# Kernel optimization log

Measured on AMD Instinct MI355X. Metric: run time of the kernel, lower is better.

Reference implementation:

```python
import jax, jax.numpy as jnp
import numpy as np
from jax import lax

T, H, K, V, O = 8192, 2048, 512, 512, 2048


def setup_inputs() -> dict:
    key = jax.random.key(0)
    ks = jax.random.split(key, 11)
    s_h = 1.0 / np.sqrt(H)
    s_v = 1.0 / np.sqrt(V)
    return {
        "hidden_state": jax.random.normal(ks[0], (T, H), jnp.float32),
        "Wq": jax.random.normal(ks[1], (H, K), jnp.float32) * s_h,
        "bq": jax.random.normal(ks[2], (K,), jnp.float32) * 0.02,
        "Wk": jax.random.normal(ks[3], (H, K), jnp.float32) * s_h,
        "bk": jax.random.normal(ks[4], (K,), jnp.float32) * 0.02,
        "Wv": jax.random.normal(ks[5], (H, V), jnp.float32) * s_h,
        "bv": jax.random.normal(ks[6], (V,), jnp.float32) * 0.02,
        "Wg": jax.random.normal(ks[7], (H, K), jnp.float32) * s_h,
        "bg": jax.random.normal(ks[8], (K,), jnp.float32) * 0.02,
        "Wo": jax.random.normal(ks[9], (V, O), jnp.float32) * s_v,
        "bo": jax.random.normal(ks[10], (O,), jnp.float32) * 0.02,
    }


def reference(hidden_state, Wq, bq, Wk, bk, Wv, bv, Wg, bg, Wo, bo):
    # Batched projections (torch Linear: x @ W^T + b; here W stored as [in,out])
    q = hidden_state @ Wq + bq                    # [T, K]
    k = jax.nn.sigmoid(hidden_state @ Wk + bk)    # [T, K]
    g = jax.nn.sigmoid(hidden_state @ Wg + bg)    # [T, K]
    v = hidden_state @ Wv + bv                    # [T, V]

    def step(state, qkvg):
        qi, ki, vi, gi = qkvg
        # state: [K, V]; gated decay per key-dim row, then outer-product write
        state = state * gi[:, None] + ki[:, None] * vi[None, :]
        out_i = qi @ state  # == state.T @ qi -> [V]
        return state, out_i

    init = jnp.zeros((K, V), hidden_state.dtype)
    final_state, outs = lax.scan(step, init, (q, k, v, g))  # outs: [T, V]
    output = outs @ Wo + bo                                  # [T, O]
    return output, final_state
```

## Files before the change

### kernel.cpp

```cpp
#include <hip/hip_runtime.h>

#define T_LEN 8192
#define H_DIM 2048
#define K_DIM 512
#define V_DIM 512
#define O_DIM 2048
#define CHUNK 64
#define NCHUNK 128

typedef short bf16x8 __attribute__((ext_vector_type(8)));
typedef float f32x4 __attribute__((ext_vector_type(4)));

typedef const __attribute__((address_space(1))) void* gptr1_t;
typedef __attribute__((address_space(3))) void* lptr3_t;

__device__ __forceinline__ float b2f(unsigned short u) {
    unsigned int i = ((unsigned int)u) << 16;
    float f;
    __builtin_memcpy(&f, &i, 4);
    return f;
}
__device__ __forceinline__ unsigned short f2b(float f) {
    unsigned int i;
    __builtin_memcpy(&i, &f, 4);
    unsigned int r = (i + 0x7FFFu + ((i >> 16) & 1u)) >> 16;
    return (unsigned short)r;
}
__device__ __forceinline__ float fw(float v) {
    return fminf(fmaxf(v, -1e30f), 1e30f);
}

#define BARX() asm volatile("s_barrier" ::: "memory")

__global__ __launch_bounds__(64) void probe_k(int* __restrict__ flag) {
    __shared__ unsigned short As[16 * 32];
    __shared__ unsigned short Bs[16 * 32];
    int tid = threadIdx.x;
    for (int idx = tid; idx < 512; idx += 64) {
        int r = idx >> 5, c = idx & 31;
        float av = (c == 0) ? (float)(r + 1) : (c == 1 ? 1.0f : 0.0f);
        float bv = (c == 0) ? 1.0f : (c == 1 ? (float)(1024 * (r + 1)) : 0.0f);
        As[r * 32 + c] = f2b(av);
        Bs[r * 32 + c] = f2b(bv);
    }
    __syncthreads();
    int ln15 = tid & 15, q4 = (tid & 63) >> 4;
    bf16x8 a = *(const bf16x8*)(As + ln15 * 32 + q4 * 8);
    bf16x8 b = *(const bf16x8*)(Bs + ln15 * 32 + q4 * 8);
    f32x4 acc = {0.f, 0.f, 0.f, 0.f};
    acc = __builtin_amdgcn_mfma_f32_16x16x32_bf16(a, b, acc, 0, 0, 0);
    bool h0 = true, h1 = true;
#pragma unroll
    for (int i = 0; i < 4; i++) {
        float e0 = (float)((q4 * 4 + i + 1) + 1024 * (ln15 + 1));
        float e1 = (float)((ln15 + 1) + 1024 * (q4 * 4 + i + 1));
        h0 = h0 && (acc[i] == e0);
        h1 = h1 && (acc[i] == e1);
    }
    unsigned long long b0 = __ballot(h0 ? 1 : 0);
    unsigned long long b1 = __ballot(h1 ? 1 : 0);
    if (tid == 0) *flag = (b0 == ~0ull) ? 0 : ((b1 == ~0ull) ? 1 : 0);
}

__global__ __launch_bounds__(256) void prep_k(const float* __restrict__ hs,
                                              unsigned short* __restrict__ hsb,
                                              const float* __restrict__ Wq,
                                              const float* __restrict__ Wk,
                                              const float* __restrict__ Wg,
                                              const float* __restrict__ Wv,
                                              const float* __restrict__ Wo,
                                              unsigned short* __restrict__ WT,
                                              unsigned short* __restrict__ WoT) {
    __shared__ unsigned short tile[32][33];
    long bid = blockIdx.x;
    int tid = threadIdx.x;
    if (bid < 8192) {
        long i = (bid * 256 + tid) * 8;
        unsigned int wd[4];
#pragma unroll
        for (int u = 0; u < 4; u++) {
            unsigned short lo = f2b(hs[i + 2 * u]);
            unsigned short hi = f2b(hs[i + 2 * u + 1]);
            wd[u] = (unsigned int)lo | ((unsigned int)hi << 16);
        }
        uint4 pk; pk.x = wd[0]; pk.y = wd[1]; pk.z = wd[2]; pk.w = wd[3];
        *(uint4*)(hsb + i) = pk;
        return;
    }
    int t = (int)(bid - 8192);
    int mat = t >> 10, tl = t & 1023;
    const float* in; unsigned short* outp; int R, C, br, bc;
    if (mat < 4) {
        in = mat == 0 ? Wq : mat == 1 ? Wk : mat == 2 ? Wg : Wv;
        outp = WT + (long)mat * 512 * H_DIM;
        R = H_DIM; C = 512; br = tl >> 4; bc = tl & 15;
    } else {
        in = Wo; outp = WoT; R = V_DIM; C = O_DIM; br = tl & 15; bc = tl >> 4;
    }
    int tc = tid & 31, tr = tid >> 5;
#pragma unroll
    for (int i = 0; i < 4; i++) {
        int r = tr + 8 * i;
        long idx = (long)(br * 32 + r) * C + bc * 32 + tc;
        tile[r][tc] = f2b(in[idx]);
    }
    __syncthreads();
#pragma unroll
    for (int i = 0; i < 4; i++) {
        int r = tr + 8 * i;
        outp[(long)(bc * 32 + r) * R + br * 32 + tc] = tile[tc][r];
    }
}

__global__ __launch_bounds__(512, 2) void proj_gemm256_k(const unsigned short* __restrict__ A,
                                                         const unsigned short* __restrict__ WT,
                                                         const float* __restrict__ bq,
                                                         const float* __restrict__ bk,
                                                         const float* __restrict__ bg,
                                                         const float* __restrict__ bv,
                                                         unsigned short* __restrict__ qb,
                                                         unsigned short* __restrict__ kb,
                                                         float* __restrict__ gb,
                                                         unsigned short* __restrict__ vT,
                                                         const int* __restrict__ flagp) {
    __shared__ unsigned short As[2][256 * 64];
    __shared__ unsigned short Bs[2][256 * 64];
    int fl = *flagp;
    int tid = threadIdx.x;
    int lane = tid & 63;
    int ln15 = lane & 15, q4 = lane >> 4;
    int w = tid >> 6;
    int wm = w >> 2, wn = w & 3;
    long m0 = (long)blockIdx.x * 256, n0 = (long)blockIdx.y * 256;

    int idx0 = tid, idx1 = 512 + tid;
    int r0_ = idx0 >> 3, r1_ = idx1 >> 3;
    int c80 = (idx0 & 7) ^ (r0_ & 7);
    int c81 = (idx1 & 7) ^ (r1_ & 7);
    int trA0 = ((r0_ >> 6) & 1) * 128 + (r0_ & 63);
    int trA1 = ((r1_ >> 6) & 1) * 128 + (r1_ & 63);
    int tcB0 = ((r0_ >> 5) & 3) * 64 + (r0_ & 31);
    int tcB1 = ((r1_ >> 5) & 3) * 64 + (r1_ & 31);
    const unsigned short* gA0 = A + (m0 + trA0) * (long)H_DIM + c80 * 8;
    const unsigned short* gA1 = A + (m0 + trA1) * (long)H_DIM + c81 * 8;
    const unsigned short* gB0 = WT + (n0 + tcB0) * (long)H_DIM + c80 * 8;
    const unsigned short* gB1 = WT + (n0 + tcB1) * (long)H_DIM + c81 * 8;
    int ld0 = idx0 * 8, ld1 = idx1 * 8;

#define STAGE_A(buf, half, ks)                                                              \
    do {                                                                                    \
        __builtin_amdgcn_global_load_lds(                                                   \
            (gptr1_t)(const void*)(gA0 + (long)(half) * 64 * H_DIM + (ks)),                 \
            (lptr3_t)(void*)(&As[buf][(half) * 8192 + ld0]), 16, 0, 0);                     \
        __builtin_amdgcn_global_load_lds(                                                   \
            (gptr1_t)(const void*)(gA1 + (long)(half) * 64 * H_DIM + (ks)),                 \
            (lptr3_t)(void*)(&As[buf][(half) * 8192 + ld1]), 16, 0, 0);                     \
    } while (0)
#define STAGE_B(buf, half, ks)                                                              \
    do {                                                                                    \
        __builtin_amdgcn_global_load_lds(                                                   \
            (gptr1_t)(const void*)(gB0 + (long)(half) * 32 * H_DIM + (ks)),                 \
            (lptr3_t)(void*)(&Bs[buf][(half) * 8192 + ld0]), 16, 0, 0);                     \
        __builtin_amdgcn_global_load_lds(                                                   \
            (gptr1_t)(const void*)(gB1 + (long)(half) * 32 * H_DIM + (ks)),                 \
            (lptr3_t)(void*)(&Bs[buf][(half) * 8192 + ld1]), 16, 0, 0);                     \
    } while (0)

    auto LDA = [&](int buf, int im, int s) -> bf16x8 {
        int row = (im >> 2) * 128 + wm * 64 + (im & 3) * 16 + ln15;
        int cb = (s * 64 + q4 * 16) ^ ((row & 7) << 4);
        return *(const bf16x8*)((const unsigned short*)As[buf] + row * 64 + (cb >> 1));
    };
    auto LDB = [&](int buf, int jn, int s) -> bf16x8 {
        int row = (jn >> 1) * 128 + wn * 32 + (jn & 1) * 16 + ln15;
        int cb = (s * 64 + q4 * 16) ^ ((row & 7) << 4);
        return *(const bf16x8*)((const unsigned short*)Bs[buf] + row * 64 + (cb >> 1));
    };

    f32x4 acc[8][4] = {};

    STAGE_A(0, 0, 0);
    STAGE_B(0, 0, 0);
    STAGE_B(0, 1, 0);
    STAGE_A(0, 1, 0);
    STAGE_A(1, 0, 64);
    STAGE_B(1, 0, 64);
    asm volatile("s_waitcnt vmcnt(4)" ::: "memory");
    BARX();

    int cur = 0;
    for (int kt = 0; kt < H_DIM; kt += 64, cur ^= 1) {
        int k1 = (kt + 64) & (H_DIM - 1);
        int k2 = (kt + 128) & (H_DIM - 1);
        bf16x8 af[4][2], blo[2][2], bhi[2][2];

#pragma unroll
        for (int i = 0; i < 4; i++) { af[i][0] = LDA(cur, i, 0); af[i][1] = LDA(cur, i, 1); }
#pragma unroll
        for (int j = 0; j < 2; j++) { blo[j][0] = LDB(cur, j, 0); blo[j][1] = LDB(cur, j, 1); }
        STAGE_B(cur ^ 1, 1, k1);
        BARX();
        __builtin_amdgcn_s_setprio(1);
#pragma unroll
        for (int i = 0; i < 4; i++)
#pragma unroll
            for (int j = 0; j < 2; j++) {
                acc[i][j] = __builtin_amdgcn_mfma_f32_16x16x32_bf16(af[i][0], blo[j][0], acc[i][j], 0, 0, 0);
                acc[i][j] = __builtin_amdgcn_mfma_f32_16x16x32_bf16(af[i][1], blo[j][1], acc[i][j], 0, 0, 0);
            }
        __builtin_amdgcn_s_setprio(0);
        BARX();

#pragma unroll
        for (int j = 0; j < 2; j++) { bhi[j][0] = LDB(cur, 2 + j, 0); bhi[j][1] = LDB(cur, 2 + j, 1); }
        STAGE_A(cur ^ 1, 1, k1);
        BARX();
        __builtin_amdgcn_s_setprio(1);
#pragma unroll
        for (int i = 0; i < 4; i++)
#pragma unroll
            for (int j = 0; j < 2; j++) {
                acc[i][2 + j] = __builtin_amdgcn_mfma_f32_16x16x32_bf16(af[i][0], bhi[j][0], acc[i][2 + j], 0, 0, 0);
                acc[i][2 + j] = __builtin_amdgcn_mfma_f32_16x16x32_bf16(af[i][1], bhi[j][1], acc[i][2 + j], 0, 0, 0);
            }
        __builtin_amdgcn_s_setprio(0);
        BARX();

#pragma unroll
        for (int i = 0; i < 4; i++) { af[i][0] = LDA(cur, 4 + i, 0); af[i][1] = LDA(cur, 4 + i, 1); }
        STAGE_A(cur, 0, k2);
        BARX();
        __builtin_amdgcn_s_setprio(1);
#pragma unroll
        for (int i = 0; i < 4; i++)
#pragma unroll
            for (int j = 0; j < 2; j++) {
                acc[4 + i][2 + j] = __builtin_amdgcn_mfma_f32_16x16x32_bf16(af[i][0], bhi[j][0], acc[4 + i][2 + j], 0, 0, 0);
                acc[4 + i][2 + j] = __builtin_amdgcn_mfma_f32_16x16x32_bf16(af[i][1], bhi[j][1], acc[4 + i][2 + j], 0, 0, 0);
            }
        __builtin_amdgcn_s_setprio(0);
        BARX();

        STAGE_B(cur, 0, k2);
        __builtin_amdgcn_s_setprio(1);
#pragma unroll
        for (int i = 0; i < 4; i++)
#pragma unroll
            for (int j = 0; j < 2; j++) {
                acc[4 + i][j] = __builtin_amdgcn_mfma_f32_16x16x32_bf16(af[i][0], blo[j][0], acc[4 + i][j], 0, 0, 0);
                acc[4 + i][j] = __builtin_amdgcn_mfma_f32_16x16x32_bf16(af[i][1], blo[j][1], acc[4 + i][j], 0, 0, 0);
            }
        __builtin_amdgcn_s_setprio(0);
        asm volatile("s_waitcnt vmcnt(4)" ::: "memory");
        BARX();
    }

    int seg = (int)(n0 >> 9);
    int nl0 = (int)(n0 & 511);
    const float* bias = seg == 0 ? bq : seg == 1 ? bk : seg == 2 ? bg : bv;

    if (seg == 3 && fl == 0) {
#pragma unroll
        for (int im = 0; im < 8; im++)
#pragma unroll
            for (int jn = 0; jn < 4; jn++) {
                int nl = nl0 + wn * 64 + (jn >> 1) * 32 + (jn & 1) * 16 + ln15;
                float bsv = bias[nl];
                long mb = m0 + wm * 128 + (im >> 2) * 64 + (im & 3) * 16 + q4 * 4;
                unsigned short h0 = f2b(fw(acc[im][jn][0] + bsv));
                unsigned short h1 = f2b(fw(acc[im][jn][1] + bsv));
                unsigned short h2 = f2b(fw(acc[im][jn][2] + bsv));
                unsigned short h3 = f2b(fw(acc[im][jn][3] + bsv));
                uint2 pk;
                pk.x = (unsigned int)h0 | ((unsigned int)h1 << 16);
                pk.y = (unsigned int)h2 | ((unsigned int)h3 << 16);
                *(uint2*)(vT + (long)nl * T_LEN + mb) = pk;
            }
    } else {
#pragma unroll
        for (int im = 0; im < 8; im++)
#pragma unroll
            for (int jn = 0; jn < 4; jn++)
#pragma unroll
                for (int ii = 0; ii < 4; ii++) {
                    int dm = fl ? ln15 : q4 * 4 + ii;
                    int dn = fl ? q4 * 4 + ii : ln15;
                    long m = m0 + wm * 128 + (im >> 2) * 64 + (im & 3) * 16 + dm;
                    int nl = nl0 + wn * 64 + (jn >> 1) * 32 + (jn & 1) * 16 + dn;
                    float v = fw(acc[im][jn][ii] + bias[nl]);
                    if (seg == 1 || seg == 2) v = 1.0f / (1.0f + __expf(-v));
                    if (seg == 0)
                        qb[m * K_DIM + nl] = f2b(v);
                    else if (seg == 1)
                        kb[m * K_DIM + nl] = f2b(v);
                    else if (seg == 2)
                        gb[m * K_DIM + nl] = v;
                    else
                        vT[(long)nl * T_LEN + m] = f2b(v);
                }
    }
#undef STAGE_A
#undef STAGE_B
}

__global__ __launch_bounds__(512, 2) void gemm256_k(const unsigned short* __restrict__ A,
                                                    const unsigned short* __restrict__ BT,
                                                    const float* __restrict__ bias,
                                                    float* __restrict__ out,
                                                    int N, int KT,
                                                    const int* __restrict__ flagp) {
    __shared__ unsigned short As[2][256 * 64];
    __shared__ unsigned short Bs[2][256 * 64];
    int fl = *flagp;
    int tid = threadIdx.x;
    int lane = tid & 63;
    int ln15 = lane & 15, q4 = lane >> 4;
    int w = tid >> 6;
    int wm = w >> 2, wn = w & 3;
    long m0 = (long)blockIdx.x * 256, n0 = (long)blockIdx.y * 256;

    int idx0 = tid, idx1 = 512 + tid;
    int r0_ = idx0 >> 3, r1_ = idx1 >> 3;
    int c80 = (idx0 & 7) ^ (r0_ & 7);
    int c81 = (idx1 & 7) ^ (r1_ & 7);
    int trA0 = ((r0_ >> 6) & 1) * 128 + (r0_ & 63);
    int trA1 = ((r1_ >> 6) & 1) * 128 + (r1_ & 63);
    int tcB0 = ((r0_ >> 5) & 3) * 64 + (r0_ & 31);
    int tcB1 = ((r1_ >> 5) & 3) * 64 + (r1_ & 31);
    const unsigned short* gA0 = A + (m0 + trA0) * (long)KT + c80 * 8;
    const unsigned short* gA1 = A + (m0 + trA1) * (long)KT + c81 * 8;
    const unsigned short* gB0 = BT + (n0 + tcB0) * (long)KT + c80 * 8;
    const unsigned short* gB1 = BT + (n0 + tcB1) * (long)KT + c81 * 8;
    int ld0 = idx0 * 8, ld1 = idx1 * 8;

#define STAGE_A(buf, half, ks)                                                              \
    do {                                                                                    \
        __builtin_amdgcn_global_load_lds(                                                   \
            (gptr1_t)(const void*)(gA0 + (long)(half) * 64 * KT + (ks)),                    \
            (lptr3_t)(void*)(&As[buf][(half) * 8192 + ld0]), 16, 0, 0);                     \
        __builtin_amdgcn_global_load_lds(                                                   \
            (gptr1_t)(const void*)(gA1 + (long)(half) * 64 * KT + (ks)),                    \
            (lptr3_t)(void*)(&As[buf][(half) * 8192 + ld1]), 16, 0, 0);                     \
    } while (0)
#define STAGE_B(buf, half, ks)                                                              \
    do {                                                                                    \
        __builtin_amdgcn_global_load_lds(                                                   \
            (gptr1_t)(const void*)(gB0 + (long)(half) * 32 * KT + (ks)),                    \
            (lptr3_t)(void*)(&Bs[buf][(half) * 8192 + ld0]), 16, 0, 0);                     \
        __builtin_amdgcn_global_load_lds(                                                   \
            (gptr1_t)(const void*)(gB1 + (long)(half) * 32 * KT + (ks)),                    \
            (lptr3_t)(void*)(&Bs[buf][(half) * 8192 + ld1]), 16, 0, 0);                     \
    } while (0)

    auto LDA = [&](int buf, int im, int s) -> bf16x8 {
        int row = (im >> 2) * 128 + wm * 64 + (im & 3) * 16 + ln15;
        int cb = (s * 64 + q4 * 16) ^ ((row & 7) << 4);
        return *(const bf16x8*)((const unsigned short*)As[buf] + row * 64 + (cb >> 1));
    };
    auto LDB = [&](int buf, int jn, int s) -> bf16x8 {
        int row = (jn >> 1) * 128 + wn * 32 + (jn & 1) * 16 + ln15;
        int cb = (s * 64 + q4 * 16) ^ ((row & 7) << 4);
        return *(const bf16x8*)((const unsigned short*)Bs[buf] + row * 64 + (cb >> 1));
    };

    f32x4 acc[8][4] = {};

    STAGE_A(0, 0, 0);
    STAGE_B(0, 0, 0);
    STAGE_B(0, 1, 0);
    STAGE_A(0, 1, 0);
    STAGE_A(1, 0, 64);
    STAGE_B(1, 0, 64);
    asm volatile("s_waitcnt vmcnt(4)" ::: "memory");
    BARX();

    int cur = 0;
    for (int kt = 0; kt < KT; kt += 64, cur ^= 1) {
        int k1 = (kt + 64) & (KT - 1);
        int k2 = (kt + 128) & (KT - 1);
        bf16x8 af[4][2], blo[2][2], bhi[2][2];

#pragma unroll
        for (int i = 0; i < 4; i++) { af[i][0] = LDA(cur, i, 0); af[i][1] = LDA(cur, i, 1); }
#pragma unroll
        for (int j = 0; j < 2; j++) { blo[j][0] = LDB(cur, j, 0); blo[j][1] = LDB(cur, j, 1); }
        STAGE_B(cur ^ 1, 1, k1);
        BARX();
        __builtin_amdgcn_s_setprio(1);
#pragma unroll
        for (int i = 0; i < 4; i++)
#pragma unroll
            for (int j = 0; j < 2; j++) {
                acc[i][j] = __builtin_amdgcn_mfma_f32_16x16x32_bf16(af[i][0], blo[j][0], acc[i][j], 0, 0, 0);
                acc[i][j] = __builtin_amdgcn_mfma_f32_16x16x32_bf16(af[i][1], blo[j][1], acc[i][j], 0, 0, 0);
            }
        __builtin_amdgcn_s_setprio(0);
        BARX();

#pragma unroll
        for (int j = 0; j < 2; j++) { bhi[j][0] = LDB(cur, 2 + j, 0); bhi[j][1] = LDB(cur, 2 + j, 1); }
        STAGE_A(cur ^ 1, 1, k1);
        BARX();
        __builtin_amdgcn_s_setprio(1);
#pragma unroll
        for (int i = 0; i < 4; i++)
#pragma unroll
            for (int j = 0; j < 2; j++) {
                acc[i][2 + j] = __builtin_amdgcn_mfma_f32_16x16x32_bf16(af[i][0], bhi[j][0], acc[i][2 + j], 0, 0, 0);
                acc[i][2 + j] = __builtin_amdgcn_mfma_f32_16x16x32_bf16(af[i][1], bhi[j][1], acc[i][2 + j], 0, 0, 0);
            }
        __builtin_amdgcn_s_setprio(0);
        BARX();

#pragma unroll
        for (int i = 0; i < 4; i++) { af[i][0] = LDA(cur, 4 + i, 0); af[i][1] = LDA(cur, 4 + i, 1); }
        STAGE_A(cur, 0, k2);
        BARX();
        __builtin_amdgcn_s_setprio(1);
#pragma unroll
        for (int i = 0; i < 4; i++)
#pragma unroll
            for (int j = 0; j < 2; j++) {
                acc[4 + i][2 + j] = __builtin_amdgcn_mfma_f32_16x16x32_bf16(af[i][0], bhi[j][0], acc[4 + i][2 + j], 0, 0, 0);
                acc[4 + i][2 + j] = __builtin_amdgcn_mfma_f32_16x16x32_bf16(af[i][1], bhi[j][1], acc[4 + i][2 + j], 0, 0, 0);
            }
        __builtin_amdgcn_s_setprio(0);
        BARX();

        STAGE_B(cur, 0, k2);
        __builtin_amdgcn_s_setprio(1);
#pragma unroll
        for (int i = 0; i < 4; i++)
#pragma unroll
            for (int j = 0; j < 2; j++) {
                acc[4 + i][j] = __builtin_amdgcn_mfma_f32_16x16x32_bf16(af[i][0], blo[j][0], acc[4 + i][j], 0, 0, 0);
                acc[4 + i][j] = __builtin_amdgcn_mfma_f32_16x16x32_bf16(af[i][1], blo[j][1], acc[4 + i][j], 0, 0, 0);
            }
        __builtin_amdgcn_s_setprio(0);
        asm volatile("s_waitcnt vmcnt(4)" ::: "memory");
        BARX();
    }

#pragma unroll
    for (int im = 0; im < 8; im++)
#pragma unroll
        for (int jn = 0; jn < 4; jn++)
#pragma unroll
            for (int ii = 0; ii < 4; ii++) {
                int dm = fl ? ln15 : q4 * 4 + ii;
                int dn = fl ? q4 * 4 + ii : ln15;
                long m = m0 + wm * 128 + (im >> 2) * 64 + (im & 3) * 16 + dm;
                long n = n0 + wn * 64 + (jn >> 1) * 32 + (jn & 1) * 16 + dn;
                out[m * N + n] = fw(acc[im][jn][ii] + bias[n]);
            }
#undef STAGE_A
#undef STAGE_B
}

__global__ __launch_bounds__(256) void cumprod_k(const float* __restrict__ g,
                                                 unsigned short* __restrict__ q,
                                                 unsigned short* __restrict__ k,
                                                 unsigned short* __restrict__ khatT,
                                                 float* __restrict__ pend) {
    int c = blockIdx.x;
    int d = blockIdx.y * 256 + threadIdx.x;
    long base = (long)c * CHUNK * K_DIM + d;
    float gv[CHUNK];
#pragma unroll
    for (int s = 0; s < CHUNK; s++) gv[s] = g[base + (long)s * K_DIM];
    float P = 1.0f;
#pragma unroll
    for (int s = 0; s < CHUNK; s++) { P = fmaxf(P * gv[s], 1e-37f); gv[s] = P; }
    pend[c * K_DIM + d] = P;
    float Pend = P;
#pragma unroll
    for (int s8 = 0; s8 < CHUNK; s8 += 8) {
        unsigned int packed[4];
#pragma unroll
        for (int u = 0; u < 8; u++) {
            int s = s8 + u;
            long idx = base + (long)s * K_DIM;
            float Pc = gv[s];
            float qv = fw(b2f(q[idx]) * Pc);
            q[idx] = f2b(qv);
            float kv = b2f(k[idx]);
            float kt = kv / Pc;
            kt = fmaxf(fminf(kt, 3e37f), -3e37f);
            k[idx] = f2b(kt);
            float ratio = Pend / Pc;
            unsigned short kh = f2b(fw(kv * ratio));
            if (u & 1)
                packed[u >> 1] |= ((unsigned int)kh) << 16;
            else
                packed[u >> 1] = kh;
        }
        uint4 pk;
        pk.x = packed[0]; pk.y = packed[1]; pk.z = packed[2]; pk.w = packed[3];
        *(uint4*)(khatT + (long)d * T_LEN + c * CHUNK + s8) = pk;
    }
}

__global__ __launch_bounds__(256) void scan_k(const unsigned short* __restrict__ khatT,
                                              const unsigned short* __restrict__ vT,
                                              const float* __restrict__ pend,
                                              unsigned short* __restrict__ ST,
                                              float* __restrict__ fstate,
                                              const int* __restrict__ flagp) {
    int fl = *flagp;
    int lane = threadIdx.x & 63, w = threadIdx.x >> 6;
    int ln15 = lane & 15, q4 = lane >> 4;
    int k0 = (blockIdx.x & 15) * 32 + (w & 1) * 16;
    int v0 = (blockIdx.x >> 4) * 32 + (w >> 1) * 16;
    f32x4 acc = {0.f, 0.f, 0.f, 0.f};
    const unsigned short* kb_ = khatT + (long)(k0 + ln15) * T_LEN + q4 * 8;
    const unsigned short* vb_ = vT + (long)(v0 + ln15) * T_LEN + q4 * 8;

    bf16x8 kf0[2], vf0[2], kf1[2], vf1[2], kf2[2], vf2[2], kf3[2], vf3[2];
    float4 pdv[4];
    float pds[4];

#define LOADSET(s, c)                                                        \
    do {                                                                     \
        long off_ = (long)(c) * CHUNK;                                       \
        kf##s[0] = *(const bf16x8*)(kb_ + off_);                             \
        kf##s[1] = *(const bf16x8*)(kb_ + off_ + 32);                        \
        vf##s[0] = *(const bf16x8*)(vb_ + off_);                             \
        vf##s[1] = *(const bf16x8*)(vb_ + off_ + 32);                        \
        if (!fl)                                                             \
            pdv[s] = *(const float4*)(pend + (c) * K_DIM + k0 + q4 * 4);     \
        else                                                                 \
            pds[s] = pend[(c) * K_DIM + k0 + ln15];                          \
    } while (0)

    LOADSET(0, 0); LOADSET(1, 1); LOADSET(2, 2); LOADSET(3, 3);

#define STEP(s, c)                                                                             \
    do {                                                                                       \
        if (!fl) {                                                                             \
            uint2 pk_;                                                                         \
            pk_.x = (unsigned int)f2b(fw(acc[0])) | ((unsigned int)f2b(fw(acc[1])) << 16);     \
            pk_.y = (unsigned int)f2b(fw(acc[2])) | ((unsigned int)f2b(fw(acc[3])) << 16);     \
            *(uint2*)(ST + ((long)(c) * V_DIM + v0 + ln15) * K_DIM + k0 + q4 * 4) = pk_;       \
            acc[0] *= pdv[s].x; acc[1] *= pdv[s].y; acc[2] *= pdv[s].z; acc[3] *= pdv[s].w;    \
        } else {                                                                               \
            ST[((long)(c) * V_DIM + v0 + q4 * 4 + 0) * K_DIM + k0 + ln15] = f2b(fw(acc[0]));   \
            ST[((long)(c) * V_DIM + v0 + q4 * 4 + 1) * K_DIM + k0 + ln15] = f2b(fw(acc[1]));   \
            ST[((long)(c) * V_DIM + v0 + q4 * 4 + 2) * K_DIM + k0 + ln15] = f2b(fw(acc[2]));   \
            ST[((long)(c) * V_DIM + v0 + q4 * 4 + 3) * K_DIM + k0 + ln15] = f2b(fw(acc[3]));   \
            acc[0] *= pds[s]; acc[1] *= pds[s]; acc[2] *= pds[s]; acc[3] *= pds[s];            \
        }                                                                                      \
        acc = __builtin_amdgcn_mfma_f32_16x16x32_bf16(kf##s[0], vf##s[0], acc, 0, 0, 0);       \
        acc = __builtin_amdgcn_mfma_f32_16x16x32_bf16(kf##s[1], vf##s[1], acc, 0, 0, 0);       \
        int cp_ = (c) + 4;                                                                     \
        if (cp_ > NCHUNK - 1) cp_ = NCHUNK - 1;                                                \
        LOADSET(s, cp_);                                                                       \
    } while (0)

    for (int c = 0; c < NCHUNK; c += 4) {
        STEP(0, c);
        STEP(1, c + 1);
        STEP(2, c + 2);
        STEP(3, c + 3);
    }
#undef STEP
#undef LOADSET

#pragma unroll
    for (int i = 0; i < 4; i++) {
        int dk = fl ? ln15 : q4 * 4 + i;
        int dv = fl ? q4 * 4 + i : ln15;
        fstate[(long)(k0 + dk) * V_DIM + v0 + dv] = fw(acc[i]);
    }
}

__global__ __launch_bounds__(256) void intra_k(const unsigned short* __restrict__ qs,
                                               const unsigned short* __restrict__ ks,
                                               const unsigned short* __restrict__ vT,
                                               const unsigned short* __restrict__ ST,
                                               unsigned short* __restrict__ outs,
                                               const int* __restrict__ flagp) {
    __shared__ unsigned short Ab[64 * 72];
    int fl = *flagp;
    long cloc = blockIdx.x >> 1;
    int c = (int)cloc, h = blockIdx.x & 1;
    int lane = threadIdx.x & 63, w = threadIdx.x >> 6;
    int ln15 = lane & 15, q4 = lane >> 4;
    long t0 = (long)c * CHUNK;

    {
        f32x4 accA[4] = {};
        for (int kk = 0; kk < K_DIM; kk += 32) {
            bf16x8 a = *(const bf16x8*)(qs + (t0 + 16 * w + ln15) * K_DIM + kk + q4 * 8);
#pragma unroll
            for (int j = 0; j < 4; j++) {
                bf16x8 b = *(const bf16x8*)(ks + (t0 + 16 * j + ln15) * K_DIM + kk + q4 * 8);
                accA[j] = __builtin_amdgcn_mfma_f32_16x16x32_bf16(a, b, accA[j], 0, 0, 0);
            }
        }
#pragma unroll
        for (int j = 0; j < 4; j++)
#pragma unroll
            for (int i = 0; i < 4; i++) {
                int dt = fl ? ln15 : q4 * 4 + i;
                int ds = fl ? q4 * 4 + i : ln15;
                int tl = 16 * w + dt;
                int s = 16 * j + ds;
                float av = (s <= tl) ? accA[j][i] : 0.0f;
                Ab[tl * 72 + s] = f2b(fw(av));
            }
    }
    __syncthreads();

    int v0 = h * 256 + w * 64;
    f32x4 acc[4][4] = {};
    for (int kk = 0; kk < K_DIM; kk += 32) {
        bf16x8 a[4], b[4];
#pragma unroll
        for (int i = 0; i < 4; i++)
            a[i] = *(const bf16x8*)(qs + (t0 + 16 * i + ln15) * K_DIM + kk + q4 * 8);
#pragma unroll
        for (int j = 0; j < 4; j++)
            b[j] = *(const bf16x8*)(ST + (cloc * V_DIM + v0 + 16 * j + ln15) * K_DIM + kk + q4 * 8);
#pragma unroll
        for (int i = 0; i < 4; i++)
#pragma unroll
            for (int j = 0; j < 4; j++)
                acc[i][j] = __builtin_amdgcn_mfma_f32_16x16x32_bf16(a[i], b[j], acc[i][j], 0, 0, 0);
    }
#pragma unroll
    for (int s0 = 0; s0 < CHUNK; s0 += 32) {
        bf16x8 a[4], b[4];
#pragma unroll
        for (int i = 0; i < 4; i++)
            a[i] = *(const bf16x8*)(Ab + (16 * i + ln15) * 72 + s0 + q4 * 8);
#pragma unroll
        for (int j = 0; j < 4; j++)
            b[j] = *(const bf16x8*)(vT + (long)(v0 + 16 * j + ln15) * T_LEN + t0 + s0 + q4 * 8);
#pragma unroll
        for (int i = 0; i < 4; i++)
#pragma unroll
            for (int j = 0; j < 4; j++)
                acc[i][j] = __builtin_amdgcn_mfma_f32_16x16x32_bf16(a[i], b[j], acc[i][j], 0, 0, 0);
    }
#pragma unroll
    for (int i = 0; i < 4; i++)
#pragma unroll
        for (int j = 0; j < 4; j++)
#pragma unroll
            for (int ii = 0; ii < 4; ii++) {
                int dt = fl ? ln15 : q4 * 4 + ii;
                int dv = fl ? q4 * 4 + ii : ln15;
                outs[(t0 + 16 * i + dt) * V_DIM + v0 + 16 * j + dv] = f2b(fw(acc[i][j][ii]));
            }
}

extern "C" void kernel_launch(void* const* d_in, const int* in_sizes, int n_in,
                              void* d_out, int out_size, void* d_ws, size_t ws_size,
                              hipStream_t stream) {
    const float* hs = (const float*)d_in[0];
    const float* Wq = (const float*)d_in[1];
    const float* bq = (const float*)d_in[2];
    const float* Wk = (const float*)d_in[3];
    const float* bk = (const float*)d_in[4];
    const float* Wv = (const float*)d_in[5];
    const float* bv = (const float*)d_in[6];
    const float* Wg = (const float*)d_in[7];
    const float* bg = (const float*)d_in[8];
    const float* Wo = (const float*)d_in[9];
    const float* bo = (const float*)d_in[10];

    float* out = (float*)d_out;

    char* ws = (char*)d_ws;
    const size_t MB = 1024 * 1024;
    unsigned short* WT = (unsigned short*)(ws + 0 * MB);
    unsigned short* outsb = (unsigned short*)(ws + 0 * MB);
    unsigned short* WoT = (unsigned short*)(ws + 8 * MB);
    unsigned short* qb = (unsigned short*)(ws + 10 * MB);
    unsigned short* kb = (unsigned short*)(ws + 18 * MB);
    unsigned short* vTb = (unsigned short*)(ws + 26 * MB);
    unsigned short* khatT = (unsigned short*)(ws + 34 * MB);
    float* pend = (float*)(ws + 42 * MB);
    int* flags = (int*)(ws + 42 * MB + 256 * 1024);
    float* gb = (float*)(ws + 44 * MB);
    unsigned short* STb = (unsigned short*)(ws + 44 * MB);
    unsigned short* hsb = (unsigned short*)(ws + 60 * MB);
    float* fsspare = (float*)(ws + 108 * MB);
    (void)ws_size; (void)in_sizes; (void)n_in;

    float* finalst =
        ((long)out_size >= (long)T_LEN * O_DIM + (long)K_DIM * V_DIM)
            ? out + (long)T_LEN * O_DIM
            : fsspare;

    dim3 b256(256);
    hipMemsetAsync(flags, 0, 16, stream);
    probe_k<<<dim3(1), dim3(64), 0, stream>>>(flags);
    prep_k<<<dim3(8192 + 5 * 1024), b256, 0, stream>>>(hs, hsb, Wq, Wk, Wg, Wv, Wo, WT, WoT);
    proj_gemm256_k<<<dim3(T_LEN / 256, 8), dim3(512), 0, stream>>>(
        hsb, WT, bq, bk, bg, bv, qb, kb, gb, vTb, flags);
    cumprod_k<<<dim3(NCHUNK, K_DIM / 256), b256, 0, stream>>>(gb, qb, kb, khatT, pend);
    scan_k<<<dim3(256), b256, 0, stream>>>(khatT, vTb, pend, STb, finalst, flags);
    intra_k<<<dim3(2 * NCHUNK), b256, 0, stream>>>(qb, kb, vTb, STb, outsb, flags);
    gemm256_k<<<dim3(T_LEN / 256, O_DIM / 256), dim3(512), 0, stream>>>(
        outsb, WoT, bo, out, O_DIM, V_DIM, flags);
}
```

Baseline: 389.7 us.

## Deepen GEMM prefetch pipeline with flat LDS addressing and coalesce khatT stores

Both 256x256 GEMM kernels now use one flat LDS array with precomputed swizzled byte offsets and incrementing global pointers, replacing per-load index arithmetic. The prologue prefetches one more half-tile, and the waits become vmcnt(8) with extra waits between phases, so more global-to-LDS loads stay in flight. The cumprod kernel stages its transposed khatT rows through a shared tile so each wave writes contiguous 128-byte row segments instead of scattered 16-byte stores. This adds wait/barrier complexity, and the pipeline depth must match the buffer reuse to stay correct.

```diff
diff --git a/kernel.cpp b/kernel.cpp
--- a/kernel.cpp
+++ b/kernel.cpp
@@ -31,6 +31,17 @@
 }
 
 #define BARX() asm volatile("s_barrier" ::: "memory")
+#define ORDER() asm volatile("" ::: "memory")
+
+#define GLDS(gp, dstByte)                                                      \
+    __builtin_amdgcn_global_load_lds((gptr1_t)(const void*)(gp),               \
+                                     (lptr3_t)(void*)((char*)lds + (dstByte)), \
+                                     16, 0, 0)
+#define STAGE2(p0, p1, dstBase)                                                \
+    do {                                                                       \
+        GLDS(p0, (dstBase) + tid * 16);                                        \
+        GLDS(p1, (dstBase) + 8192 + tid * 16);                                 \
+    } while (0)
 
 __global__ __launch_bounds__(64) void probe_k(int* __restrict__ flag) {
     __shared__ unsigned short As[16 * 32];
@@ -123,8 +134,7 @@
                                                          float* __restrict__ gb,
                                                          unsigned short* __restrict__ vT,
                                                          const int* __restrict__ flagp) {
-    __shared__ unsigned short As[2][256 * 64];
-    __shared__ unsigned short Bs[2][256 * 64];
+    __shared__ short lds[65536];
     int fl = *flagp;
     int tid = threadIdx.x;
     int lane = tid & 63;
@@ -132,6 +142,10 @@
     int w = tid >> 6;
     int wm = w >> 2, wn = w & 3;
     long m0 = (long)blockIdx.x * 256, n0 = (long)blockIdx.y * 256;
+
+    unsigned slot = ((unsigned)(q4 * 16)) ^ ((unsigned)((ln15 & 7) << 4));
+    unsigned aoff0 = (unsigned)(wm * 8192 + ln15 * 128) + slot;
+    unsigned boff0 = 65536u + (unsigned)(wn * 4096 + ln15 * 128) + slot;
 
     int idx0 = tid, idx1 = 512 + tid;
     int r0_ = idx0 >> 3, r1_ = idx1 >> 3;
@@ -141,64 +155,52 @@
     int trA1 = ((r1_ >> 6) & 1) * 128 + (r1_ & 63);
     int tcB0 = ((r0_ >> 5) & 3) * 64 + (r0_ & 31);
     int tcB1 = ((r1_ >> 5) & 3) * 64 + (r1_ & 31);
-    const unsigned short* gA0 = A + (m0 + trA0) * (long)H_DIM + c80 * 8;
-    const unsigned short* gA1 = A + (m0 + trA1) * (long)H_DIM + c81 * 8;
-    const unsigned short* gB0 = WT + (n0 + tcB0) * (long)H_DIM + c80 * 8;
-    const unsigned short* gB1 = WT + (n0 + tcB1) * (long)H_DIM + c81 * 8;
-    int ld0 = idx0 * 8, ld1 = idx1 * 8;
-
-#define STAGE_A(buf, half, ks)                                                              \
-    do {                                                                                    \
-        __builtin_amdgcn_global_load_lds(                                                   \
-            (gptr1_t)(const void*)(gA0 + (long)(half) * 64 * H_DIM + (ks)),                 \
-            (lptr3_t)(void*)(&As[buf][(half) * 8192 + ld0]), 16, 0, 0);                     \
-        __builtin_amdgcn_global_load_lds(                                                   \
-            (gptr1_t)(const void*)(gA1 + (long)(half) * 64 * H_DIM + (ks)),                 \
-            (lptr3_t)(void*)(&As[buf][(half) * 8192 + ld1]), 16, 0, 0);                     \
-    } while (0)
-#define STAGE_B(buf, half, ks)                                                              \
-    do {                                                                                    \
-        __builtin_amdgcn_global_load_lds(                                                   \
-            (gptr1_t)(const void*)(gB0 + (long)(half) * 32 * H_DIM + (ks)),                 \
-            (lptr3_t)(void*)(&Bs[buf][(half) * 8192 + ld0]), 16, 0, 0);                     \
-        __builtin_amdgcn_global_load_lds(                                                   \
-            (gptr1_t)(const void*)(gB1 + (long)(half) * 32 * H_DIM + (ks)),                 \
-            (lptr3_t)(void*)(&Bs[buf][(half) * 8192 + ld1]), 16, 0, 0);                     \
-    } while (0)
-
-    auto LDA = [&](int buf, int im, int s) -> bf16x8 {
-        int row = (im >> 2) * 128 + wm * 64 + (im & 3) * 16 + ln15;
-        int cb = (s * 64 + q4 * 16) ^ ((row & 7) << 4);
-        return *(const bf16x8*)((const unsigned short*)As[buf] + row * 64 + (cb >> 1));
-    };
-    auto LDB = [&](int buf, int jn, int s) -> bf16x8 {
-        int row = (jn >> 1) * 128 + wn * 32 + (jn & 1) * 16 + ln15;
-        int cb = (s * 64 + q4 * 16) ^ ((row & 7) << 4);
-        return *(const bf16x8*)((const unsigned short*)Bs[buf] + row * 64 + (cb >> 1));
-    };
+    const unsigned short* pAlo0 = A + (m0 + trA0) * (long)H_DIM + c80 * 8;
+    const unsigned short* pAlo1 = A + (m0 + trA1) * (long)H_DIM + c81 * 8;
+    const unsigned short* pAhi0 = pAlo0 + 64 * H_DIM;
+    const unsigned short* pAhi1 = pAlo1 + 64 * H_DIM;
+    const unsigned short* pBlo0 = WT + (n0 + tcB0) * (long)H_DIM + c80 * 8;
+    const unsigned short* pBlo1 = WT + (n0 + tcB1) * (long)H_DIM + c81 * 8;
+    const unsigned short* pBhi0 = pBlo0 + 32 * H_DIM;
+    const unsigned short* pBhi1 = pBlo1 + 32 * H_DIM;
 
     f32x4 acc[8][4] = {};
 
-    STAGE_A(0, 0, 0);
-    STAGE_B(0, 0, 0);
-    STAGE_B(0, 1, 0);
-    STAGE_A(0, 1, 0);
-    STAGE_A(1, 0, 64);
-    STAGE_B(1, 0, 64);
-    asm volatile("s_waitcnt vmcnt(4)" ::: "memory");
+    STAGE2(pAlo0, pAlo1, 0);
+    STAGE2(pBlo0, pBlo1, 65536);
+    ORDER();
+    STAGE2(pBhi0, pBhi1, 65536 + 16384);
+    STAGE2(pAhi0, pAhi1, 16384);
+    ORDER();
+    pAlo0 += 64; pAlo1 += 64; pBlo0 += 64; pBlo1 += 64;
+    STAGE2(pAlo0, pAlo1, 32768);
+    STAGE2(pBlo0, pBlo1, 65536 + 32768);
+    ORDER();
+    pAlo0 += 64; pAlo1 += 64; pBlo0 += 64; pBlo1 += 64;
+    pAhi0 += 64; pAhi1 += 64; pBhi0 += 64; pBhi1 += 64;
+    asm volatile("s_waitcnt vmcnt(8)" ::: "memory");
     BARX();
 
     int cur = 0;
+    const char* L = (const char*)lds;
     for (int kt = 0; kt < H_DIM; kt += 64, cur ^= 1) {
-        int k1 = (kt + 64) & (H_DIM - 1);
-        int k2 = (kt + 128) & (H_DIM - 1);
+        int nxt = cur ^ 1;
+        unsigned bufb = (unsigned)cur << 15;
+        unsigned ab0 = aoff0 + bufb, ab1 = ab0 ^ 64u;
+        unsigned bb0 = boff0 + bufb, bb1 = bb0 ^ 64u;
         bf16x8 af[4][2], blo[2][2], bhi[2][2];
 
 #pragma unroll
-        for (int i = 0; i < 4; i++) { af[i][0] = LDA(cur, i, 0); af[i][1] = LDA(cur, i, 1); }
-#pragma unroll
-        for (int j = 0; j < 2; j++) { blo[j][0] = LDB(cur, j, 0); blo[j][1] = LDB(cur, j, 1); }
-        STAGE_B(cur ^ 1, 1, k1);
+        for (int i = 0; i < 4; i++) {
+            af[i][0] = *(const bf16x8*)(L + ab0 + i * 2048);
+            af[i][1] = *(const bf16x8*)(L + ab1 + i * 2048);
+        }
+#pragma unroll
+        for (int j = 0; j < 2; j++) {
+            blo[j][0] = *(const bf16x8*)(L + bb0 + j * 2048);
+            blo[j][1] = *(const bf16x8*)(L + bb1 + j * 2048);
+        }
+        STAGE2(pBhi0, pBhi1, 65536 + nxt * 32768 + 16384);
         BARX();
         __builtin_amdgcn_s_setprio(1);
 #pragma unroll
@@ -209,11 +211,15 @@
                 acc[i][j] = __builtin_amdgcn_mfma_f32_16x16x32_bf16(af[i][1], blo[j][1], acc[i][j], 0, 0, 0);
             }
         __builtin_amdgcn_s_setprio(0);
-        BARX();
-
-#pragma unroll
-        for (int j = 0; j < 2; j++) { bhi[j][0] = LDB(cur, 2 + j, 0); bhi[j][1] = LDB(cur, 2 + j, 1); }
-        STAGE_A(cur ^ 1, 1, k1);
+        asm volatile("s_waitcnt vmcnt(8)" ::: "memory");
+        BARX();
+
+#pragma unroll
+        for (int j = 0; j < 2; j++) {
+            bhi[j][0] = *(const bf16x8*)(L + bb0 + 16384 + j * 2048);
+            bhi[j][1] = *(const bf16x8*)(L + bb1 + 16384 + j * 2048);
+        }
+        STAGE2(pAhi0, pAhi1, nxt * 32768 + 16384);
         BARX();
         __builtin_amdgcn_s_setprio(1);
 #pragma unroll
@@ -224,11 +230,15 @@
                 acc[i][2 + j] = __builtin_amdgcn_mfma_f32_16x16x32_bf16(af[i][1], bhi[j][1], acc[i][2 + j], 0, 0, 0);
             }
         __builtin_amdgcn_s_setprio(0);
-        BARX();
-
-#pragma unroll
-        for (int i = 0; i < 4; i++) { af[i][0] = LDA(cur, 4 + i, 0); af[i][1] = LDA(cur, 4 + i, 1); }
-        STAGE_A(cur, 0, k2);
+        asm volatile("s_waitcnt vmcnt(8)" ::: "memory");
+        BARX();
+
+#pragma unroll
+        for (int i = 0; i < 4; i++) {
+            af[i][0] = *(const bf16x8*)(L + ab0 + 16384 + i * 2048);
+            af[i][1] = *(const bf16x8*)(L + ab1 + 16384 + i * 2048);
+        }
+        STAGE2(pAlo0, pAlo1, cur * 32768);
         BARX();
         __builtin_amdgcn_s_setprio(1);
 #pragma unroll
@@ -241,7 +251,7 @@
         __builtin_amdgcn_s_setprio(0);
         BARX();
 
-        STAGE_B(cur, 0, k2);
+        STAGE2(pBlo0, pBlo1, 65536 + cur * 32768);
         __builtin_amdgcn_s_setprio(1);
 #pragma unroll
         for (int i = 0; i < 4; i++)
@@ -251,8 +261,11 @@
                 acc[4 + i][j] = __builtin_amdgcn_mfma_f32_16x16x32_bf16(af[i][1], blo[j][1], acc[4 + i][j], 0, 0, 0);
             }
         __builtin_amdgcn_s_setprio(0);
-        asm volatile("s_waitcnt vmcnt(4)" ::: "memory");
-        BARX();
+        asm volatile("s_waitcnt vmcnt(8)" ::: "memory");
+        BARX();
+
+        pAlo0 += 64; pAlo1 += 64; pAhi0 += 64; pAhi1 += 64;
+        pBlo0 += 64; pBlo1 += 64; pBhi0 += 64; pBhi1 += 64;
     }
 
     int seg = (int)(n0 >> 9);
@@ -299,8 +312,6 @@
                         vT[(long)nl * T_LEN + m] = f2b(v);
                 }
     }
-#undef STAGE_A
-#undef STAGE_B
 }
 
 __global__ __launch_bounds__(512, 2) void gemm256_k(const unsigned short* __restrict__ A,
@@ -309,8 +320,7 @@
                                                     float* __restrict__ out,
                                                     int N, int KT,
                                                     const int* __restrict__ flagp) {
-    __shared__ unsigned short As[2][256 * 64];
-    __shared__ unsigned short Bs[2][256 * 64];
+    __shared__ short lds[65536];
     int fl = *flagp;
     int tid = threadIdx.x;
     int lane = tid & 63;
@@ -318,6 +328,10 @@
     int w = tid >> 6;
     int wm = w >> 2, wn = w & 3;
     long m0 = (long)blockIdx.x * 256, n0 = (long)blockIdx.y * 256;
+
+    unsigned slot = ((unsigned)(q4 * 16)) ^ ((unsigned)((ln15 & 7) << 4));
+    unsigned aoff0 = (unsigned)(wm * 8192 + ln15 * 128) + slot;
+    unsigned boff0 = 65536u + (unsigned)(wn * 4096 + ln15 * 128) + slot;
 
     int idx0 = tid, idx1 = 512 + tid;
     int r0_ = idx0 >> 3, r1_ = idx1 >> 3;
@@ -327,64 +341,52 @@
     int trA1 = ((r1_ >> 6) & 1) * 128 + (r1_ & 63);
     int tcB0 = ((r0_ >> 5) & 3) * 64 + (r0_ & 31);
     int tcB1 = ((r1_ >> 5) & 3) * 64 + (r1_ & 31);
-    const unsigned short* gA0 = A + (m0 + trA0) * (long)KT + c80 * 8;
-    const unsigned short* gA1 = A + (m0 + trA1) * (long)KT + c81 * 8;
-    const unsigned short* gB0 = BT + (n0 + tcB0) * (long)KT + c80 * 8;
-    const unsigned short* gB1 = BT + (n0 + tcB1) * (long)KT + c81 * 8;
-    int ld0 = idx0 * 8, ld1 = idx1 * 8;
-
-#define STAGE_A(buf, half, ks)                                                              \
-    do {                                                                                    \
-        __builtin_amdgcn_global_load_lds(                                                   \
-            (gptr1_t)(const void*)(gA0 + (long)(half) * 64 * KT + (ks)),                    \
-            (lptr3_t)(void*)(&As[buf][(half) * 8192 + ld0]), 16, 0, 0);                     \
-        __builtin_amdgcn_global_load_lds(                                                   \
-            (gptr1_t)(const void*)(gA1 + (long)(half) * 64 * KT + (ks)),                    \
-            (lptr3_t)(void*)(&As[buf][(half) * 8192 + ld1]), 16, 0, 0);                     \
-    } while (0)
-#define STAGE_B(buf, half, ks)                                                              \
-    do {                                                                                    \
-        __builtin_amdgcn_global_load_lds(                                                   \
-            (gptr1_t)(const void*)(gB0 + (long)(half) * 32 * KT + (ks)),                    \
-            (lptr3_t)(void*)(&Bs[buf][(half) * 8192 + ld0]), 16, 0, 0);                     \
-        __builtin_amdgcn_global_load_lds(                                                   \
-            (gptr1_t)(const void*)(gB1 + (long)(half) * 32 * KT + (ks)),                    \
-            (lptr3_t)(void*)(&Bs[buf][(half) * 8192 + ld1]), 16, 0, 0);                     \
-    } while (0)
-
-    auto LDA = [&](int buf, int im, int s) -> bf16x8 {
-        int row = (im >> 2) * 128 + wm * 64 + (im & 3) * 16 + ln15;
-        int cb = (s * 64 + q4 * 16) ^ ((row & 7) << 4);
-        return *(const bf16x8*)((const unsigned short*)As[buf] + row * 64 + (cb >> 1));
-    };
-    auto LDB = [&](int buf, int jn, int s) -> bf16x8 {
-        int row = (jn >> 1) * 128 + wn * 32 + (jn & 1) * 16 + ln15;
-        int cb = (s * 64 + q4 * 16) ^ ((row & 7) << 4);
-        return *(const bf16x8*)((const unsigned short*)Bs[buf] + row * 64 + (cb >> 1));
-    };
+    const unsigned short* pAlo0 = A + (m0 + trA0) * (long)KT + c80 * 8;
+    const unsigned short* pAlo1 = A + (m0 + trA1) * (long)KT + c81 * 8;
+    const unsigned short* pAhi0 = pAlo0 + 64 * KT;
+    const unsigned short* pAhi1 = pAlo1 + 64 * KT;
+    const unsigned short* pBlo0 = BT + (n0 + tcB0) * (long)KT + c80 * 8;
+    const unsigned short* pBlo1 = BT + (n0 + tcB1) * (long)KT + c81 * 8;
+    const unsigned short* pBhi0 = pBlo0 + 32 * KT;
+    const unsigned short* pBhi1 = pBlo1 + 32 * KT;
 
     f32x4 acc[8][4] = {};
 
-    STAGE_A(0, 0, 0);
-    STAGE_B(0, 0, 0);
-    STAGE_B(0, 1, 0);
-    STAGE_A(0, 1, 0);
-    STAGE_A(1, 0, 64);
-    STAGE_B(1, 0, 64);
-    asm volatile("s_waitcnt vmcnt(4)" ::: "memory");
+    STAGE2(pAlo0, pAlo1, 0);
+    STAGE2(pBlo0, pBlo1, 65536);
+    ORDER();
+    STAGE2(pBhi0, pBhi1, 65536 + 16384);
+    STAGE2(pAhi0, pAhi1, 16384);
+    ORDER();
+    pAlo0 += 64; pAlo1 += 64; pBlo0 += 64; pBlo1 += 64;
+    STAGE2(pAlo0, pAlo1, 32768);
+    STAGE2(pBlo0, pBlo1, 65536 + 32768);
+    ORDER();
+    pAlo0 += 64; pAlo1 += 64; pBlo0 += 64; pBlo1 += 64;
+    pAhi0 += 64; pAhi1 += 64; pBhi0 += 64; pBhi1 += 64;
+    asm volatile("s_waitcnt vmcnt(8)" ::: "memory");
     BARX();
 
     int cur = 0;
+    const char* L = (const char*)lds;
     for (int kt = 0; kt < KT; kt += 64, cur ^= 1) {
-        int k1 = (kt + 64) & (KT - 1);
-        int k2 = (kt + 128) & (KT - 1);
+        int nxt = cur ^ 1;
+        unsigned bufb = (unsigned)cur << 15;
+        unsigned ab0 = aoff0 + bufb, ab1 = ab0 ^ 64u;
+        unsigned bb0 = boff0 + bufb, bb1 = bb0 ^ 64u;
         bf16x8 af[4][2], blo[2][2], bhi[2][2];
 
 #pragma unroll
-        for (int i = 0; i < 4; i++) { af[i][0] = LDA(cur, i, 0); af[i][1] = LDA(cur, i, 1); }
-#pragma unroll
-        for (int j = 0; j < 2; j++) { blo[j][0] = LDB(cur, j, 0); blo[j][1] = LDB(cur, j, 1); }
-        STAGE_B(cur ^ 1, 1, k1);
+        for (int i = 0; i < 4; i++) {
+            af[i][0] = *(const bf16x8*)(L + ab0 + i * 2048);
+            af[i][1] = *(const bf16x8*)(L + ab1 + i * 2048);
+        }
+#pragma unroll
+        for (int j = 0; j < 2; j++) {
+            blo[j][0] = *(const bf16x8*)(L + bb0 + j * 2048);
+            blo[j][1] = *(const bf16x8*)(L + bb1 + j * 2048);
+        }
+        STAGE2(pBhi0, pBhi1, 65536 + nxt * 32768 + 16384);
         BARX();
         __builtin_amdgcn_s_setprio(1);
 #pragma unroll
@@ -395,11 +397,15 @@
                 acc[i][j] = __builtin_amdgcn_mfma_f32_16x16x32_bf16(af[i][1], blo[j][1], acc[i][j], 0, 0, 0);
             }
         __builtin_amdgcn_s_setprio(0);
-        BARX();
-
-#pragma unroll
-        for (int j = 0; j < 2; j++) { bhi[j][0] = LDB(cur, 2 + j, 0); bhi[j][1] = LDB(cur, 2 + j, 1); }
-        STAGE_A(cur ^ 1, 1, k1);
+        asm volatile("s_waitcnt vmcnt(8)" ::: "memory");
+        BARX();
+
+#pragma unroll
+        for (int j = 0; j < 2; j++) {
+            bhi[j][0] = *(const bf16x8*)(L + bb0 + 16384 + j * 2048);
+            bhi[j][1] = *(const bf16x8*)(L + bb1 + 16384 + j * 2048);
+        }
+        STAGE2(pAhi0, pAhi1, nxt * 32768 + 16384);
         BARX();
         __builtin_amdgcn_s_setprio(1);
 #pragma unroll
@@ -410,11 +416,15 @@
                 acc[i][2 + j] = __builtin_amdgcn_mfma_f32_16x16x32_bf16(af[i][1], bhi[j][1], acc[i][2 + j], 0, 0, 0);
             }
         __builtin_amdgcn_s_setprio(0);
-        BARX();
-
-#pragma unroll
-        for (int i = 0; i < 4; i++) { af[i][0] = LDA(cur, 4 + i, 0); af[i][1] = LDA(cur, 4 + i, 1); }
-        STAGE_A(cur, 0, k2);
+        asm volatile("s_waitcnt vmcnt(8)" ::: "memory");
+        BARX();
+
+#pragma unroll
+        for (int i = 0; i < 4; i++) {
+            af[i][0] = *(const bf16x8*)(L + ab0 + 16384 + i * 2048);
+            af[i][1] = *(const bf16x8*)(L + ab1 + 16384 + i * 2048);
+        }
+        STAGE2(pAlo0, pAlo1, cur * 32768);
         BARX();
         __builtin_amdgcn_s_setprio(1);
 #pragma unroll
@@ -427,7 +437,7 @@
         __builtin_amdgcn_s_setprio(0);
         BARX();
 
-        STAGE_B(cur, 0, k2);
+        STAGE2(pBlo0, pBlo1, 65536 + cur * 32768);
         __builtin_amdgcn_s_setprio(1);
 #pragma unroll
         for (int i = 0; i < 4; i++)
@@ -437,8 +447,11 @@
                 acc[4 + i][j] = __builtin_amdgcn_mfma_f32_16x16x32_bf16(af[i][1], blo[j][1], acc[4 + i][j], 0, 0, 0);
             }
         __builtin_amdgcn_s_setprio(0);
-        asm volatile("s_waitcnt vmcnt(4)" ::: "memory");
-        BARX();
+        asm volatile("s_waitcnt vmcnt(8)" ::: "memory");
+        BARX();
+
+        pAlo0 += 64; pAlo1 += 64; pAhi0 += 64; pAhi1 += 64;
+        pBlo0 += 64; pBlo1 += 64; pBhi0 += 64; pBhi1 += 64;
     }
 
 #pragma unroll
@@ -453,8 +466,6 @@
                 long n = n0 + wn * 64 + (jn >> 1) * 32 + (jn & 1) * 16 + dn;
                 out[m * N + n] = fw(acc[im][jn][ii] + bias[n]);
             }
-#undef STAGE_A
-#undef STAGE_B
 }
 
 __global__ __launch_bounds__(256) void cumprod_k(const float* __restrict__ g,
@@ -462,8 +473,11 @@
                                                  unsigned short* __restrict__ k,
                                                  unsigned short* __restrict__ khatT,
                                                  float* __restrict__ pend) {
+    __shared__ unsigned short tile[256][80];
     int c = blockIdx.x;
-    int d = blockIdx.y * 256 + threadIdx.x;
+    int half = blockIdx.y;
+    int tid = threadIdx.x;
+    int d = half * 256 + tid;
     long base = (long)c * CHUNK * K_DIM + d;
     float gv[CHUNK];
 #pragma unroll
@@ -496,7 +510,16 @@
         }
         uint4 pk;
         pk.x = packed[0]; pk.y = packed[1]; pk.z = packed[2]; pk.w = packed[3];
-        *(uint4*)(khatT + (long)d * T_LEN + c * CHUNK + s8) = pk;
+        *(uint4*)&tile[tid][s8] = pk;
+    }
+    __syncthreads();
+    int wv = tid >> 6, l = tid & 63;
+    int colb = (l & 7) * 8;
+#pragma unroll
+    for (int j = 0; j < 8; j++) {
+        int row = wv * 64 + j * 8 + (l >> 3);
+        uint4 pk = *(const uint4*)&tile[row][colb];
+        *(uint4*)(khatT + (long)(half * 256 + row) * T_LEN + c * CHUNK + colb) = pk;
     }
 }
 
```

Measured after the change: 391.3 us. No clear change (+0.4%).
